# Kernel tuning notes

Hardware: AMD Instinct MI355X
Metric: run time of the kernel (lower is better)

The kernel has to match this reference:

```python
import jax, jax.numpy as jnp
import numpy as np


def _rot(phi, theta, omega):
    # PennyLane Rot = RZ(omega) @ RY(theta) @ RZ(phi)
    ct = jnp.cos(0.5 * theta)
    st = jnp.sin(0.5 * theta)
    a = jnp.exp(-0.5j * (phi + omega))  # complex64 since inputs are float32
    b = jnp.exp(0.5j * (phi - omega))
    return jnp.stack([
        jnp.stack([a * ct, -b * st]),
        jnp.stack([jnp.conj(b) * st, jnp.conj(a) * ct]),
    ])


def _apply_1q(psi, U, wire):
    # psi: (2,2,2) complex; apply 2x2 U on `wire`
    psi = jnp.tensordot(U, psi, axes=([1], [wire]))
    return jnp.moveaxis(psi, 0, wire)


def _cnot(psi, c, t):
    # CNOT with control c, target t (static ints)
    t_ = t - (1 if t > c else 0)
    a = jnp.take(psi, 0, axis=c)
    b = jnp.flip(jnp.take(psi, 1, axis=c), axis=t_)
    return jnp.stack([a, b], axis=c)


def _circuit(x3, w):
    # x3: (3,) angles; w: (L, 3, 3) StronglyEntanglingLayers weights
    # AngleEmbedding(rotation='Y') on |000>: product of RY(x_i)|0>
    c = jnp.cos(0.5 * x3)
    s = jnp.sin(0.5 * x3)
    psi = (jnp.stack([c[0], s[0]])[:, None, None]
           * jnp.stack([c[1], s[1]])[None, :, None]
           * jnp.stack([c[2], s[2]])[None, None, :]).astype(jnp.complex64)
    L = w.shape[0]
    for l in range(L):
        for q in range(3):
            psi = _apply_1q(psi, _rot(w[l, q, 0], w[l, q, 1], w[l, q, 2]), q)
        r = (l % 2) + 1  # PennyLane default ranges for 3 wires: (l % (n-1)) + 1
        for q in range(3):
            psi = _cnot(psi, q, (q + r) % 3)
    p = (psi * jnp.conj(psi)).real
    p0 = p.sum((1, 2))
    p1 = p.sum((0, 2))
    p2 = p.sum((0, 1))
    return jnp.stack([p0[0] - p0[1], p1[0] - p1[1], p2[0] - p2[1]])


# vmap over blocks, then timesteps (both x and theta), then batch (theta shared)
_circ_full = jax.vmap(jax.vmap(jax.vmap(_circuit, (0, 0)), (0, 0)), (0, None))


def _forward(x, theta):
    # x: (B, T, D); theta: (T, n_layers, n_blocks, L, 3, 3)
    B, T, D = x.shape
    nb = D // 3
    n_layers = theta.shape[1]
    # 'multiple' mode rewiring: block i reads [3i-1, 3i+1, 3i+3] mod D
    idx = (jnp.arange(nb)[:, None] * 3 + jnp.array([-1, 1, 3])) % D
    # layer 0: 'first' mode = contiguous 3-wide blocks
    H = _circ_full(x.reshape(B, T, nb, 3), theta[:, 0]).reshape(B, T, D)
    for l in range(1, n_layers):
        H = _circ_full(H[..., idx], theta[:, l]).reshape(B, T, D)
    return H


def setup_inputs() -> dict:
    key = jax.random.key(0)
    k1, k2 = jax.random.split(key)
    B, T, D = 128, 64, 96
    n_layers, n_blocks, vqc_depth = 3, D // 3, 2
    x = jax.random.normal(k1, (B, T, D), dtype=jnp.float32)
    theta = 0.01 * jax.random.normal(k2, (T, n_layers, n_blocks, vqc_depth, 3, 3), dtype=jnp.float32)
    return {"x": x, "theta": theta}


def reference(x, theta):
    return _forward(x, theta)
```

## Files before the change

kernel.cpp:

```cpp
#include <hip/hip_runtime.h>


#define T_DIM 64
#define D_DIM 96
#define NB 32
#define NLAYER 3
#define ROTS_PER_T (NLAYER * 6 * NB)
#define THETA_PER_T (NLAYER * NB * 18)

typedef float v2f __attribute__((ext_vector_type(2)));

__device__ __forceinline__ void rot_pk(v2f psi[8], float4 r, int bit) {
    const v2f Xb = {r.x, r.x};
    const v2f Yn = {-r.y, r.y};
    const v2f Ub = {r.z, r.z};
    const v2f Vn = {r.w, -r.w};
#pragma unroll
    for (int k = 0; k < 8; ++k) {
        if (k & bit) continue;
        v2f p0 = psi[k], p1 = psi[k | bit];
        v2f s0 = {p0.y, p0.x}, s1 = {p1.y, p1.x};
        v2f o0 = Xb * p0 + Yn * s0 - Ub * p1 + Vn * s1;
        v2f o1 = Ub * p0 + Vn * s0 + Xb * p1 - Yn * s1;
        psi[k] = o0; psi[k | bit] = o1;
    }
}

__device__ __forceinline__ void cnot(v2f psi[8], int cb, int tb) {
#pragma unroll
    for (int k = 0; k < 8; ++k) {
        if ((k & cb) && !(k & tb)) {
            v2f tmp = psi[k]; psi[k] = psi[k | tb]; psi[k | tb] = tmp;
        }
    }
}

__global__ __launch_bounds__(256, 4) void qnn_fused(const float* __restrict__ x,
                                                    const float* __restrict__ theta,
                                                    float* __restrict__ out) {
    __shared__ float4 rotS[ROTS_PER_T];

    const int tid = threadIdx.x;
    const int t  = blockIdx.x >> 4;
    const int bg = blockIdx.x & 15;
    const int pr = tid >> 5;
    const int i  = tid & 31;
    const int b  = bg * 8 + pr;
    const int bt = b * T_DIM + t;

    const float* xp = x + (size_t)bt * D_DIM + 3 * i;
    const float a0 = xp[0], a1 = xp[1], a2 = xp[2];

    const float* gth = theta + (size_t)t * THETA_PER_T;
    for (int idx = tid; idx < ROTS_PER_T; idx += 256) {
        int l   = idx / 192;
        int rem = idx - l * 192;
        int j   = rem >> 5;
        int ii  = rem & 31;
        const float* p = gth + ((l * NB + ii) * 6 + j) * 3;
        float phi = p[0], tht = p[1], omg = p[2];
        float st, ct; __sincosf(0.5f * tht, &st, &ct);
        float sa, ca; __sincosf(-0.5f * (phi + omg), &sa, &ca);
        float sb, cb; __sincosf(0.5f * (phi - omg), &sb, &cb);
        rotS[idx] = make_float4(ca * ct, sa * ct, cb * st, sb * st);
    }
    __syncthreads();

    float ang0 = a0, ang1 = a1, ang2 = a2;
    float res0 = 0.f, res1 = 0.f, res2 = 0.f;
#pragma unroll
    for (int l = 0; l < NLAYER; ++l) {
        if (l) {
            ang0 = __shfl(res2, (i + 31) & 31, 32);
            ang1 = res1;
            ang2 = __shfl(res0, (i + 1) & 31, 32);
        }
        float4 rr[6];
#pragma unroll
        for (int j = 0; j < 6; ++j) rr[j] = rotS[l * 192 + j * 32 + i];

        float c0, s0, c1, s1, c2, s2;
        __sincosf(0.5f * ang0, &s0, &c0);
        __sincosf(0.5f * ang1, &s1, &c1);
        __sincosf(0.5f * ang2, &s2, &c2);
        v2f psi[8];
        {
            float cc = c0 * c1, cs = c0 * s1, sc = s0 * c1, ss = s0 * s1;
            psi[0] = (v2f){cc * c2, 0.f}; psi[1] = (v2f){cc * s2, 0.f};
            psi[2] = (v2f){cs * c2, 0.f}; psi[3] = (v2f){cs * s2, 0.f};
            psi[4] = (v2f){sc * c2, 0.f}; psi[5] = (v2f){sc * s2, 0.f};
            psi[6] = (v2f){ss * c2, 0.f}; psi[7] = (v2f){ss * s2, 0.f};
        }
#pragma unroll
        for (int vl = 0; vl < 2; ++vl) {
#pragma unroll
            for (int q = 0; q < 3; ++q) rot_pk(psi, rr[vl * 3 + q], 4 >> q);
            int rngr = vl + 1;
#pragma unroll
            for (int q = 0; q < 3; ++q) cnot(psi, 4 >> q, 4 >> ((q + rngr) % 3));
        }
        float pb[8];
#pragma unroll
        for (int k = 0; k < 8; ++k) {
            v2f sq = psi[k] * psi[k];
            pb[k] = sq.x + sq.y;
        }
        float s01 = pb[0] + pb[1], s23 = pb[2] + pb[3];
        float s45 = pb[4] + pb[5], s67 = pb[6] + pb[7];
        float q0 = pb[0] + pb[4], q1 = pb[1] + pb[5];
        float q2 = pb[2] + pb[6], q3 = pb[3] + pb[7];
        res0 = (s01 + s23) - (s45 + s67);
        res1 = (q0 + q1) - (q2 + q3);
        res2 = (q0 + q2) - (q1 + q3);
    }

    float* op = out + (size_t)bt * D_DIM + 3 * i;
    op[0] = res0; op[1] = res1; op[2] = res2;
}

extern "C" void kernel_launch(void* const* d_in, const int* in_sizes, int n_in,
                              void* d_out, int out_size, void* d_ws, size_t ws_size,
                              hipStream_t stream) {
    const float* x = (const float*)d_in[0];
    const float* theta = (const float*)d_in[1];
    float* out = (float*)d_out;

    qnn_fused<<<64 * 16, 256, 0, stream>>>(x, theta, out);
}
```

Before: 13.53 us.

## Process two batch rows per thread and fold first rotation layer into product state

Each thread now evaluates two batch elements, packed in a split real/imaginary v2f layout so packed FMA covers both samples, and the grid is halved. The first variational layer's single-qubit rotations are applied analytically to the product-state factors before the tensor product, which skips three full 8-amplitude gate applications. The CNOT sequences are written out explicitly. In exchange, register pressure per thread roughly doubles (launch bounds lowered to 2 waves), there are fewer blocks, and the per-block theta precompute is amortized over twice the work.

```diff
diff --git a/kernel.cpp b/kernel.cpp
--- a/kernel.cpp
+++ b/kernel.cpp
@@ -10,46 +10,71 @@
 
 typedef float v2f __attribute__((ext_vector_type(2)));
 
-__device__ __forceinline__ void rot_pk(v2f psi[8], float4 r, int bit) {
-    const v2f Xb = {r.x, r.x};
-    const v2f Yn = {-r.y, r.y};
-    const v2f Ub = {r.z, r.z};
-    const v2f Vn = {r.w, -r.w};
+struct c2 { v2f re, im; };
+
+__device__ __forceinline__ c2 cmul2(c2 a, c2 b) {
+    c2 r;
+    r.re = a.re * b.re - a.im * b.im;
+    r.im = a.re * b.im + a.im * b.re;
+    return r;
+}
+
+__device__ __forceinline__ void apply1q(float4 r, v2f c, v2f s, c2& e0, c2& e1) {
+    e0.re = r.x * c - r.z * s;
+    e0.im = r.y * c - r.w * s;
+    e1.re = r.z * c + r.x * s;
+    e1.im = -(r.w * c + r.y * s);
+}
+
+__device__ __forceinline__ void gate_pk(c2 psi[8], float4 r, int bit) {
+    const v2f X = {r.x, r.x}, Y = {r.y, r.y}, U = {r.z, r.z}, V = {r.w, r.w};
 #pragma unroll
     for (int k = 0; k < 8; ++k) {
         if (k & bit) continue;
-        v2f p0 = psi[k], p1 = psi[k | bit];
-        v2f s0 = {p0.y, p0.x}, s1 = {p1.y, p1.x};
-        v2f o0 = Xb * p0 + Yn * s0 - Ub * p1 + Vn * s1;
-        v2f o1 = Ub * p0 + Vn * s0 + Xb * p1 - Yn * s1;
+        c2 p0 = psi[k], p1 = psi[k | bit], o0, o1;
+        o0.re = X * p0.re - Y * p0.im - U * p1.re + V * p1.im;
+        o0.im = Y * p0.re + X * p0.im - V * p1.re - U * p1.im;
+        o1.re = U * p0.re + V * p0.im + X * p1.re + Y * p1.im;
+        o1.im = U * p0.im - V * p0.re + X * p1.im - Y * p1.re;
         psi[k] = o0; psi[k | bit] = o1;
     }
 }
 
-__device__ __forceinline__ void cnot(v2f psi[8], int cb, int tb) {
+__device__ __forceinline__ void cnot_c2(c2 psi[8], int cb, int tb) {
 #pragma unroll
     for (int k = 0; k < 8; ++k) {
         if ((k & cb) && !(k & tb)) {
-            v2f tmp = psi[k]; psi[k] = psi[k | tb]; psi[k | tb] = tmp;
+            c2 tmp = psi[k]; psi[k] = psi[k | tb]; psi[k | tb] = tmp;
         }
     }
 }
 
-__global__ __launch_bounds__(256, 4) void qnn_fused(const float* __restrict__ x,
+__device__ __forceinline__ void sc2(v2f a, v2f& s, v2f& c) {
+    float sx, cx, sy, cy;
+    __sincosf(0.5f * a.x, &sx, &cx);
+    __sincosf(0.5f * a.y, &sy, &cy);
+    s = (v2f){sx, sy}; c = (v2f){cx, cy};
+}
+
+__global__ __launch_bounds__(256, 2) void qnn_fused(const float* __restrict__ x,
                                                     const float* __restrict__ theta,
                                                     float* __restrict__ out) {
     __shared__ float4 rotS[ROTS_PER_T];
 
     const int tid = threadIdx.x;
-    const int t  = blockIdx.x >> 4;
-    const int bg = blockIdx.x & 15;
+    const int t  = blockIdx.x >> 3;
+    const int bg = blockIdx.x & 7;
     const int pr = tid >> 5;
     const int i  = tid & 31;
-    const int b  = bg * 8 + pr;
-    const int bt = b * T_DIM + t;
+    const int b0 = bg * 16 + pr;
+    const int bt0 = b0 * T_DIM + t;
+    const int bt1 = bt0 + 8 * T_DIM;
 
-    const float* xp = x + (size_t)bt * D_DIM + 3 * i;
-    const float a0 = xp[0], a1 = xp[1], a2 = xp[2];
+    const float* xp0 = x + (size_t)bt0 * D_DIM + 3 * i;
+    const float* xp1 = x + (size_t)bt1 * D_DIM + 3 * i;
+    v2f ang0 = {xp0[0], xp1[0]};
+    v2f ang1 = {xp0[1], xp1[1]};
+    v2f ang2 = {xp0[2], xp1[2]};
 
     const float* gth = theta + (size_t)t * THETA_PER_T;
     for (int idx = tid; idx < ROTS_PER_T; idx += 256) {
@@ -66,56 +91,57 @@
     }
     __syncthreads();
 
-    float ang0 = a0, ang1 = a1, ang2 = a2;
-    float res0 = 0.f, res1 = 0.f, res2 = 0.f;
+    v2f res0 = {0.f, 0.f}, res1 = {0.f, 0.f}, res2 = {0.f, 0.f};
 #pragma unroll
     for (int l = 0; l < NLAYER; ++l) {
         if (l) {
-            ang0 = __shfl(res2, (i + 31) & 31, 32);
+            int lm = (i + 31) & 31, lp = (i + 1) & 31;
+            ang0 = (v2f){__shfl(res2.x, lm, 32), __shfl(res2.y, lm, 32)};
             ang1 = res1;
-            ang2 = __shfl(res0, (i + 1) & 31, 32);
+            ang2 = (v2f){__shfl(res0.x, lp, 32), __shfl(res0.y, lp, 32)};
         }
         float4 rr[6];
 #pragma unroll
         for (int j = 0; j < 6; ++j) rr[j] = rotS[l * 192 + j * 32 + i];
 
-        float c0, s0, c1, s1, c2, s2;
-        __sincosf(0.5f * ang0, &s0, &c0);
-        __sincosf(0.5f * ang1, &s1, &c1);
-        __sincosf(0.5f * ang2, &s2, &c2);
-        v2f psi[8];
-        {
-            float cc = c0 * c1, cs = c0 * s1, sc = s0 * c1, ss = s0 * s1;
-            psi[0] = (v2f){cc * c2, 0.f}; psi[1] = (v2f){cc * s2, 0.f};
-            psi[2] = (v2f){cs * c2, 0.f}; psi[3] = (v2f){cs * s2, 0.f};
-            psi[4] = (v2f){sc * c2, 0.f}; psi[5] = (v2f){sc * s2, 0.f};
-            psi[6] = (v2f){ss * c2, 0.f}; psi[7] = (v2f){ss * s2, 0.f};
-        }
+        v2f c0, s0, c1, s1, c2v, s2v;
+        sc2(ang0, s0, c0); sc2(ang1, s1, c1); sc2(ang2, s2v, c2v);
+
+        c2 A0, A1, B0, B1, C0, C1;
+        apply1q(rr[0], c0, s0, A0, A1);
+        apply1q(rr[1], c1, s1, B0, B1);
+        apply1q(rr[2], c2v, s2v, C0, C1);
+        c2 T00 = cmul2(A0, B0), T01 = cmul2(A0, B1);
+        c2 T10 = cmul2(A1, B0), T11 = cmul2(A1, B1);
+        c2 psi[8];
+        psi[0] = cmul2(T00, C0); psi[1] = cmul2(T00, C1);
+        psi[2] = cmul2(T01, C0); psi[3] = cmul2(T01, C1);
+        psi[4] = cmul2(T10, C0); psi[5] = cmul2(T10, C1);
+        psi[6] = cmul2(T11, C0); psi[7] = cmul2(T11, C1);
+
+        cnot_c2(psi, 4, 2); cnot_c2(psi, 2, 1); cnot_c2(psi, 1, 4);
+
+        gate_pk(psi, rr[3], 4); gate_pk(psi, rr[4], 2); gate_pk(psi, rr[5], 1);
+
+        cnot_c2(psi, 4, 1); cnot_c2(psi, 2, 4); cnot_c2(psi, 1, 2);
+
+        v2f pb[8];
 #pragma unroll
-        for (int vl = 0; vl < 2; ++vl) {
-#pragma unroll
-            for (int q = 0; q < 3; ++q) rot_pk(psi, rr[vl * 3 + q], 4 >> q);
-            int rngr = vl + 1;
-#pragma unroll
-            for (int q = 0; q < 3; ++q) cnot(psi, 4 >> q, 4 >> ((q + rngr) % 3));
-        }
-        float pb[8];
-#pragma unroll
-        for (int k = 0; k < 8; ++k) {
-            v2f sq = psi[k] * psi[k];
-            pb[k] = sq.x + sq.y;
-        }
-        float s01 = pb[0] + pb[1], s23 = pb[2] + pb[3];
-        float s45 = pb[4] + pb[5], s67 = pb[6] + pb[7];
-        float q0 = pb[0] + pb[4], q1 = pb[1] + pb[5];
-        float q2 = pb[2] + pb[6], q3 = pb[3] + pb[7];
+        for (int k = 0; k < 8; ++k)
+            pb[k] = psi[k].re * psi[k].re + psi[k].im * psi[k].im;
+        v2f s01 = pb[0] + pb[1], s23 = pb[2] + pb[3];
+        v2f s45 = pb[4] + pb[5], s67 = pb[6] + pb[7];
+        v2f q0 = pb[0] + pb[4], q1 = pb[1] + pb[5];
+        v2f q2 = pb[2] + pb[6], q3 = pb[3] + pb[7];
         res0 = (s01 + s23) - (s45 + s67);
         res1 = (q0 + q1) - (q2 + q3);
         res2 = (q0 + q2) - (q1 + q3);
     }
 
-    float* op = out + (size_t)bt * D_DIM + 3 * i;
-    op[0] = res0; op[1] = res1; op[2] = res2;
+    float* op0 = out + (size_t)bt0 * D_DIM + 3 * i;
+    float* op1 = out + (size_t)bt1 * D_DIM + 3 * i;
+    op0[0] = res0.x; op0[1] = res1.x; op0[2] = res2.x;
+    op1[0] = res0.y; op1[1] = res1.y; op1[2] = res2.y;
 }
 
 extern "C" void kernel_launch(void* const* d_in, const int* in_sizes, int n_in,
@@ -125,5 +151,5 @@
     const float* theta = (const float*)d_in[1];
     float* out = (float*)d_out;
 
-    qnn_fused<<<64 * 16, 256, 0, stream>>>(x, theta, out);
+    qnn_fused<<<64 * 8, 256, 0, stream>>>(x, theta, out);
 }
```

Measured after the change: 11.46 us. 1.18x faster.
